# Kernel tuning notes

Hardware: AMD Instinct MI355X
Metric: run time of the kernel (lower is better)

## Reference

```python
import jax, jax.numpy as jnp
import numpy as np

D = 2048
H = 16
DH = D // H
S = 8192
EPS = 1e-6  # flax LayerNorm default


def _ln(x, g, b):
    m = jnp.mean(x, axis=-1, keepdims=True)
    v = jnp.var(x, axis=-1, keepdims=True)
    return (x - m) * jax.lax.rsqrt(v + EPS) * g + b


def setup_inputs() -> dict:
    key = jax.random.key(0)
    ks = jax.random.split(key, 12)
    sd = 1.0 / np.sqrt(D)
    sdf = 1.0 / np.sqrt(4 * D)
    return {
        "self_tok": jax.random.normal(ks[0], (D,), jnp.float32),
        "all_toks": jax.random.normal(ks[1], (S, D), jnp.float32),
        "wq": jax.random.normal(ks[2], (D, D), jnp.float32) * sd,
        "bq": jnp.zeros((D,), jnp.float32),
        "wk": jax.random.normal(ks[3], (D, D), jnp.float32) * sd,
        "bk": jnp.zeros((D,), jnp.float32),
        "wv": jax.random.normal(ks[4], (D, D), jnp.float32) * sd,
        "bv": jnp.zeros((D,), jnp.float32),
        "wo": jax.random.normal(ks[5], (D, D), jnp.float32) * sd,
        "bo": jnp.zeros((D,), jnp.float32),
        "g1": jnp.ones((D,), jnp.float32),
        "b1": jnp.zeros((D,), jnp.float32),
        "g2": jnp.ones((D,), jnp.float32),
        "b2": jnp.zeros((D,), jnp.float32),
        "w_ffn1": jax.random.normal(ks[6], (D, 4 * D), jnp.float32) * sd,
        "b_ffn1": jnp.zeros((4 * D,), jnp.float32),
        "w_ffn2": jax.random.normal(ks[7], (4 * D, D), jnp.float32) * sdf,
        "b_ffn2": jnp.zeros((D,), jnp.float32),
    }


def reference(self_tok, all_toks, wq, bq, wk, bk, wv, bv, wo, bo,
              g1, b1, g2, b2, w_ffn1, b_ffn1, w_ffn2, b_ffn2):
    # pre-norm (norm1 applied to both query token and KV tokens)
    n_self = _ln(self_tok, g1, b1)            # [D]
    n_all = _ln(all_toks, g1, b1)             # [S, D]
    q = (n_self @ wq + bq).reshape(H, DH)     # [H, Dh]
    k = (n_all @ wk + bk).reshape(S, H, DH)   # [S, H, Dh]
    v = (n_all @ wv + bv).reshape(S, H, DH)
    scale = DH ** -0.5
    scores = jnp.einsum('hd,shd->hs', q, k) * scale   # [H, S]
    attn = jax.nn.softmax(scores, axis=-1)
    out = jnp.einsum('hs,shd->hd', attn, v).reshape(D)
    out = out @ wo + bo
    x = self_tok + out
    ffn = jax.nn.gelu(_ln(x, g2, b2) @ w_ffn1 + b_ffn1) @ w_ffn2 + b_ffn2
    return x + ffn
```

## Files before the change

kernel.cpp:

```cpp
#include <hip/hip_runtime.h>

#define DEV __device__ __forceinline__

constexpr int D  = 2048;
constexpr int H  = 16;
constexpr int DH = 128;
constexpr int S  = 8192;
constexpr float EPS = 1e-6f;
constexpr float SCALE = 0.08838834764831845f;
constexpr float M0 = 8.0f;

typedef unsigned short ushortv4 __attribute__((ext_vector_type(4)));
typedef short bf16x8 __attribute__((ext_vector_type(8)));
typedef float f32x4 __attribute__((ext_vector_type(4)));

DEV float bf2f(unsigned short u){ return __uint_as_float(((unsigned int)u) << 16); }
DEV unsigned short f2bf(float f){
  unsigned int x = __float_as_uint(f);
  unsigned int r = x + 0x7fffu + ((x >> 16) & 1u);
  return (unsigned short)(r >> 16);
}

DEV float gelu(float x){
  float x3 = x * x * x;
  return 0.5f * x * (1.f + tanhf(0.7978845608028654f * (x + 0.044715f * x3)));
}

template<int NW>
DEV void block_sum2(float& a, float& b, float* buf){
  #pragma unroll
  for(int o = 32; o; o >>= 1){ a += __shfl_xor(a, o); b += __shfl_xor(b, o); }
  const int w = threadIdx.x >> 6;
  if((threadIdx.x & 63) == 0){ buf[w] = a; buf[NW + w] = b; }
  __syncthreads();
  a = buf[0]; b = buf[NW];
  #pragma unroll
  for(int i = 1; i < NW; i++){ a += buf[i]; b += buf[NW + i]; }
}

__global__ __launch_bounds__(256) void k_pre(const float* __restrict__ at,
    const float* __restrict__ g1, const float* __restrict__ b1,
    unsigned short* __restrict__ nall,
    const float* __restrict__ st, const float* __restrict__ wq,
    float* __restrict__ qpart){
  const int t = threadIdx.x;
  const int bid = blockIdx.x;
  const int w = t >> 6, l = t & 63;
  if(bid < 2048){
    const size_t s = (size_t)bid * 4 + w;
    const float4* row4 = (const float4*)(at + s * D);
    float4 a[8];
    float sum = 0.f, sq = 0.f;
    #pragma unroll
    for(int k = 0; k < 8; k++){
      a[k] = row4[l + 64 * k];
      sum += a[k].x + a[k].y + a[k].z + a[k].w;
      sq  += a[k].x*a[k].x + a[k].y*a[k].y + a[k].z*a[k].z + a[k].w*a[k].w;
    }
    #pragma unroll
    for(int o = 32; o; o >>= 1){ sum += __shfl_xor(sum, o); sq += __shfl_xor(sq, o); }
    const float m = sum * (1.f / D);
    const float r = rsqrtf(sq * (1.f / D) - m * m + EPS);
    const float4* g4 = (const float4*)g1;
    const float4* b4 = (const float4*)b1;
    ushortv4* nst = (ushortv4*)(nall + s * D);
    #pragma unroll
    for(int k = 0; k < 8; k++){
      const int j4 = l + 64 * k;
      float4 gg = g4[j4], bb = b4[j4];
      ushortv4 o4;
      o4[0] = f2bf((a[k].x - m) * r * gg.x + bb.x);
      o4[1] = f2bf((a[k].y - m) * r * gg.y + bb.y);
      o4[2] = f2bf((a[k].z - m) * r * gg.z + bb.z);
      o4[3] = f2bf((a[k].w - m) * r * gg.w + bb.w);
      nst[j4] = o4;
    }
  } else {
    __shared__ float buf[8];
    __shared__ float ns_s[32];
    const int qb_ = bid - 2048;
    const int jc = qb_ >> 3, ic = qb_ & 7;
    const int j0 = jc * 32;
    float4 a = ((const float4*)st)[t], c = ((const float4*)st)[t + 256];
    float sum = a.x + a.y + a.z + a.w + c.x + c.y + c.z + c.w;
    float sq  = a.x*a.x + a.y*a.y + a.z*a.z + a.w*a.w
              + c.x*c.x + c.y*c.y + c.z*c.z + c.w*c.w;
    block_sum2<4>(sum, sq, buf);
    const float m = sum * (1.f / D);
    const float r = rsqrtf(sq * (1.f / D) - m * m + EPS);
    if(t < 32){
      int j = j0 + t;
      ns_s[t] = (st[j] - m) * r * g1[j] + b1[j];
    }
    __syncthreads();
    const int i = ic * 256 + t;
    float acc = 0.f;
    #pragma unroll 8
    for(int jj = 0; jj < 32; jj++)
      acc = fmaf(ns_s[jj], wq[(size_t)(j0 + jj) * D + i], acc);
    qpart[(size_t)jc * D + i] = acc;
  }
}

__global__ __launch_bounds__(256) void k_qred(const float* __restrict__ qpart,
    const float* __restrict__ bq, float* __restrict__ q){
  const int i = blockIdx.x * 256 + threadIdx.x;
  float s = bq[i];
  #pragma unroll 8
  for(int p = 0; p < 64; p++) s += qpart[(size_t)p * D + i];
  q[i] = s;
}

__global__ __launch_bounds__(256) void k_wkq(const float* __restrict__ wk,
    const float* __restrict__ bk, const float* __restrict__ q,
    unsigned short* __restrict__ wkqT, float* __restrict__ qb){
  const int t = threadIdx.x;
  const int w = t >> 6, l = t & 63;
  const int row = blockIdx.x * 2 + (w >> 1);
  const int hw = w & 1;
  if(row > D) return;
  const float* src = (row < D) ? (wk + (size_t)row * D) : bk;
  const float4* s4 = (const float4*)src;
  const float4* q4 = (const float4*)q;
  float ph[4];
  #pragma unroll
  for(int kk = 0; kk < 4; kk++){
    const int kc = hw * 4 + kk;
    float4 a = s4[l + 64 * kc];
    float4 qq = q4[l + 64 * kc];
    ph[kk] = a.x*qq.x + a.y*qq.y + a.z*qq.z + a.w*qq.w;
  }
  #pragma unroll
  for(int o = 1; o < 32; o <<= 1){
    #pragma unroll
    for(int kk = 0; kk < 4; kk++) ph[kk] += __shfl_xor(ph[kk], o);
  }
  if((l & 31) == 0){
    const int hb = l >> 5;
    #pragma unroll
    for(int kk = 0; kk < 4; kk++){
      const int h = 2 * (hw * 4 + kk) + hb;
      if(row < D) wkqT[(size_t)h * D + row] = f2bf(ph[kk]);
      else        qb[h] = ph[kk];
    }
  }
}

__global__ __launch_bounds__(512) void k_scores(
    const unsigned short* __restrict__ nall,
    const unsigned short* __restrict__ wkqT,
    const float* __restrict__ qb,
    float* __restrict__ p,
    float* __restrict__ zb){
  __shared__ f32x4 cred[8][64];
  const int t = threadIdx.x;
  const int w = t >> 6, lane = t & 63;
  const int s0 = blockIdx.x * 16;
  const int m16 = lane & 15;
  const int kg  = lane >> 4;
  f32x4 c = {0.f, 0.f, 0.f, 0.f};
  const int kbase = w * 256 + kg * 8;
  const unsigned short* aptr = wkqT + (size_t)m16 * D + kbase;
  const unsigned short* bptr = nall + (size_t)(s0 + m16) * D + kbase;
  #pragma unroll
  for(int kk = 0; kk < 8; kk++){
    bf16x8 av = *(const bf16x8*)(aptr + kk * 32);
    bf16x8 bv = *(const bf16x8*)(bptr + kk * 32);
    c = __builtin_amdgcn_mfma_f32_16x16x32_bf16(av, bv, c, 0, 0, 0);
  }
  cred[w][lane] = c;
  __syncthreads();
  if(w == 0){
    f32x4 cs_ = cred[0][lane];
    #pragma unroll
    for(int pg = 1; pg < 8; pg++){
      f32x4 cp = cred[pg][lane];
      cs_[0] += cp[0]; cs_[1] += cp[1]; cs_[2] += cp[2]; cs_[3] += cp[3];
    }
    float pv[4];
    #pragma unroll
    for(int rg = 0; rg < 4; rg++)
      pv[rg] = __expf((cs_[rg] + qb[kg * 4 + rg]) * SCALE - M0);
    float4 st4;
    st4.x = pv[0]; st4.y = pv[1]; st4.z = pv[2]; st4.w = pv[3];
    *(float4*)(p + (size_t)(s0 + m16) * H + kg * 4) = st4;
    #pragma unroll
    for(int rg = 0; rg < 4; rg++){
      float e = pv[rg];
      #pragma unroll
      for(int o = 1; o < 16; o <<= 1) e += __shfl_xor(e, o);
      pv[rg] = e;
    }
    if(m16 == 0){
      float4 bz;
      bz.x = pv[0]; bz.y = pv[1]; bz.z = pv[2]; bz.w = pv[3];
      *(float4*)(zb + (size_t)blockIdx.x * H + kg * 4) = bz;
    }
  }
}

__global__ __launch_bounds__(256) void k_actx(const unsigned short* __restrict__ nall,
    const float* __restrict__ p, float* __restrict__ part){
  __shared__ float pl[64][16];
  const int jc = blockIdx.x, sc = blockIdx.y, t = threadIdx.x;
  const int s0 = sc * 64;
  #pragma unroll
  for(int u = 0; u < 4; u++){
    int idx = t + 256 * u;
    int ss = idx >> 4, hh = idx & 15;
    pl[ss][hh] = p[(size_t)(s0 + ss) * H + hh];
  }
  __syncthreads();
  const int j = jc * 512 + 2 * t;
  float acc[16][2];
  #pragma unroll
  for(int h = 0; h < 16; h++){ acc[h][0] = 0.f; acc[h][1] = 0.f; }
  for(int s8 = 0; s8 < 8; s8++){
    unsigned int nv[8];
    #pragma unroll
    for(int e = 0; e < 8; e++)
      nv[e] = *(const unsigned int*)(nall + (size_t)(s0 + s8 * 8 + e) * D + j);
    #pragma unroll
    for(int e = 0; e < 8; e++){
      const int ss = s8 * 8 + e;
      float n0 = bf2f((unsigned short)(nv[e] & 0xffffu));
      float n1 = bf2f((unsigned short)(nv[e] >> 16));
      const float4* pp = (const float4*)pl[ss];
      #pragma unroll
      for(int hq = 0; hq < 4; hq++){
        float4 p4 = pp[hq];
        acc[hq*4+0][0] = fmaf(p4.x, n0, acc[hq*4+0][0]);
        acc[hq*4+0][1] = fmaf(p4.x, n1, acc[hq*4+0][1]);
        acc[hq*4+1][0] = fmaf(p4.y, n0, acc[hq*4+1][0]);
        acc[hq*4+1][1] = fmaf(p4.y, n1, acc[hq*4+1][1]);
        acc[hq*4+2][0] = fmaf(p4.z, n0, acc[hq*4+2][0]);
        acc[hq*4+2][1] = fmaf(p4.z, n1, acc[hq*4+2][1]);
        acc[hq*4+3][0] = fmaf(p4.w, n0, acc[hq*4+3][0]);
        acc[hq*4+3][1] = fmaf(p4.w, n1, acc[hq*4+3][1]);
      }
    }
  }
  #pragma unroll
  for(int h = 0; h < 16; h++){
    float2 st2; st2.x = acc[h][0]; st2.y = acc[h][1];
    *(float2*)(part + ((size_t)sc * 16 + h) * D + j) = st2;
  }
}

__global__ __launch_bounds__(256) void k_wv(const float* __restrict__ part,
    const float* __restrict__ zb, const float* __restrict__ wv,
    float* __restrict__ part_wv){
  __shared__ float zred[16][16];
  __shared__ float ihz_s;
  __shared__ float a4[4][64];
  __shared__ float as[64];
  __shared__ float red2[2][128];
  const int h = blockIdx.x, jc = blockIdx.y, t = threadIdx.x;
  const int j0 = jc * 64;
  {
    const int hh = t & 15, u = t >> 4;
    float s = 0.f;
    #pragma unroll
    for(int k = 0; k < 32; k++) s += zb[(size_t)(u + 16 * k) * 16 + hh];
    zred[u][hh] = s;
  }
  __syncthreads();
  if(t == 0){
    float z = 0.f;
    #pragma unroll
    for(int u = 0; u < 16; u++) z += zred[u][h];
    ihz_s = 1.f / z;
  }
  const int jq = t & 63, qq = t >> 6;
  float s_ = 0.f;
  #pragma unroll
  for(int u = 0; u < 32; u++){
    int sc = qq * 32 + u;
    s_ += part[((size_t)sc * 16 + h) * D + j0 + jq];
  }
  a4[qq][jq] = s_;
  __syncthreads();
  if(t < 64) as[t] = (a4[0][t] + a4[1][t] + a4[2][t] + a4[3][t]) * ihz_s;
  __syncthreads();
  const int hf = t >> 7, il = t & 127;
  const int i = h * DH + il;
  float acc = 0.f;
  #pragma unroll
  for(int u = 0; u < 32; u++){
    int jj = hf * 32 + u;
    acc = fmaf(as[jj], wv[(size_t)(j0 + jj) * D + i], acc);
  }
  red2[hf][il] = acc;
  __syncthreads();
  if(t < 128) part_wv[(size_t)jc * D + h * DH + t] = red2[0][t] + red2[1][t];
}

__global__ __launch_bounds__(256) void k_wo(const float* __restrict__ part_wv,
    const float* __restrict__ bv, const float* __restrict__ wo,
    float* __restrict__ part_wo){
  __shared__ float oa[32];
  const int ic = blockIdx.x, jc = blockIdx.y, t = threadIdx.x;
  const int j0 = jc * 32;
  if(t < 32){
    float s = bv[j0 + t];
    #pragma unroll
    for(int pg = 0; pg < 32; pg++) s += part_wv[(size_t)pg * D + j0 + t];
    oa[t] = s;
  }
  __syncthreads();
  const int i = ic * 256 + t;
  float acc = 0.f;
  #pragma unroll
  for(int jj = 0; jj < 32; jj++)
    acc = fmaf(oa[jj], wo[(size_t)(j0 + jj) * D + i], acc);
  part_wo[(size_t)jc * D + i] = acc;
}

__global__ __launch_bounds__(256) void k_x(const float* __restrict__ self_tok,
    const float* __restrict__ bo, const float* __restrict__ part_wo,
    float* __restrict__ x, float* __restrict__ xstat){
  __shared__ float buf[8];
  const int b = blockIdx.x, t = threadIdx.x;
  const int i = b * 256 + t;
  float s = self_tok[i] + bo[i];
  #pragma unroll 8
  for(int pg = 0; pg < 64; pg++) s += part_wo[(size_t)pg * D + i];
  x[i] = s;
  float sq = s * s;
  block_sum2<4>(s, sq, buf);
  if(t == 0){ xstat[2 * b] = s; xstat[2 * b + 1] = sq; }
}

__global__ __launch_bounds__(256) void k_f1(const float* __restrict__ x,
    const float* __restrict__ xstat, const float* __restrict__ g2,
    const float* __restrict__ b2, const float* __restrict__ w1,
    float* __restrict__ part_f1){
  __shared__ float xs[128];
  __shared__ float stat[2];
  const int oc = blockIdx.x, jc = blockIdx.y, t = threadIdx.x;
  if(t == 0){
    float s1 = 0.f, s2 = 0.f;
    #pragma unroll
    for(int pg = 0; pg < 8; pg++){ s1 += xstat[2 * pg]; s2 += xstat[2 * pg + 1]; }
    float m = s1 * (1.f / D);
    stat[0] = m;
    stat[1] = rsqrtf(s2 * (1.f / D) - m * m + EPS);
  }
  __syncthreads();
  if(t < 128){
    int j = jc * 128 + t;
    xs[t] = (x[j] - stat[0]) * stat[1] * g2[j] + b2[j];
  }
  __syncthreads();
  const int o = oc * 256 + t;
  float acc = 0.f;
  #pragma unroll 8
  for(int jj = 0; jj < 128; jj++)
    acc = fmaf(xs[jj], w1[(size_t)(jc * 128 + jj) * (4 * D) + o], acc);
  part_f1[(size_t)jc * (4 * D) + o] = acc;
}

__global__ __launch_bounds__(256) void k_f2(const float* __restrict__ part_f1,
    const float* __restrict__ b_f1, const float* __restrict__ w2,
    float* __restrict__ part_f2){
  __shared__ float hs[128];
  const int ic = blockIdx.x, jc = blockIdx.y, t = threadIdx.x;
  if(t < 128){
    int jh = jc * 128 + t;
    float s = b_f1[jh];
    #pragma unroll
    for(int pg = 0; pg < 16; pg++) s += part_f1[(size_t)pg * (4 * D) + jh];
    hs[t] = gelu(s);
  }
  __syncthreads();
  const int i = ic * 256 + t;
  float acc = 0.f;
  #pragma unroll 8
  for(int jj = 0; jj < 128; jj++)
    acc = fmaf(hs[jj], w2[(size_t)(jc * 128 + jj) * D + i], acc);
  part_f2[(size_t)jc * D + i] = acc;
}

__global__ __launch_bounds__(256) void k_final(const float* __restrict__ part_f2,
    const float* __restrict__ x, const float* __restrict__ b_f2,
    float* __restrict__ out){
  const int i = blockIdx.x * 256 + threadIdx.x;
  float s = x[i] + b_f2[i];
  #pragma unroll 8
  for(int jc = 0; jc < 64; jc++) s += part_f2[(size_t)jc * D + i];
  out[i] = s;
}

extern "C" void kernel_launch(void* const* d_in, const int* in_sizes, int n_in,
                              void* d_out, int out_size, void* d_ws, size_t ws_size,
                              hipStream_t stream){
  const float* self_tok = (const float*)d_in[0];
  const float* all_toks = (const float*)d_in[1];
  const float* wq = (const float*)d_in[2];
  const float* bq = (const float*)d_in[3];
  const float* wk = (const float*)d_in[4];
  const float* bk = (const float*)d_in[5];
  const float* wv = (const float*)d_in[6];
  const float* bv = (const float*)d_in[7];
  const float* wo = (const float*)d_in[8];
  const float* bo = (const float*)d_in[9];
  const float* g1 = (const float*)d_in[10];
  const float* b1 = (const float*)d_in[11];
  const float* g2 = (const float*)d_in[12];
  const float* b2 = (const float*)d_in[13];
  const float* w1 = (const float*)d_in[14];
  const float* b_f1 = (const float*)d_in[15];
  const float* w2 = (const float*)d_in[16];
  const float* b_f2 = (const float*)d_in[17];
  float* out = (float*)d_out;

  char* wptr = (char*)d_ws;
  auto alloc = [&](size_t bytes) -> void* {
    void* pt = (void*)wptr;
    wptr += (bytes + 255) & ~(size_t)255;
    return pt;
  };
  unsigned short* n_all = (unsigned short*)alloc((size_t)S * D * 2);
  unsigned short* wkqT  = (unsigned short*)alloc((size_t)H * D * 2);
  float* pbuf      = (float*)alloc((size_t)S * H * 4);
  float* zb        = (float*)alloc((size_t)(S / 16) * H * 4);
  float* qpart     = (float*)alloc((size_t)64 * D * 4);
  float* q         = (float*)alloc((size_t)D * 4);
  float* qb        = (float*)alloc(64);
  float* part_actx = (float*)alloc((size_t)128 * H * D * 4);
  float* part_wv   = (float*)alloc((size_t)32 * D * 4);
  float* part_wo   = (float*)alloc((size_t)64 * D * 4);
  float* xbuf      = (float*)alloc((size_t)D * 4);
  float* xstat     = (float*)alloc(64);
  float* part_f1   = (float*)alloc((size_t)16 * 4 * D * 4);
  float* part_f2   = (float*)alloc((size_t)64 * D * 4);

  k_pre<<<2048 + 512, 256, 0, stream>>>(all_toks, g1, b1, n_all, self_tok, wq, qpart);
  k_qred<<<8, 256, 0, stream>>>(qpart, bq, q);
  k_wkq<<<(D / 2) + 1, 256, 0, stream>>>(wk, bk, q, wkqT, qb);
  k_scores<<<S / 16, 512, 0, stream>>>(n_all, wkqT, qb, pbuf, zb);
  k_actx<<<dim3(4, 128), 256, 0, stream>>>(n_all, pbuf, part_actx);
  k_wv<<<dim3(16, 32), 256, 0, stream>>>(part_actx, zb, wv, part_wv);
  k_wo<<<dim3(8, 64), 256, 0, stream>>>(part_wv, bv, wo, part_wo);
  k_x<<<8, 256, 0, stream>>>(self_tok, bo, part_wo, xbuf, xstat);
  k_f1<<<dim3(32, 16), 256, 0, stream>>>(xbuf, xstat, g2, b2, w1, part_f1);
  k_f2<<<dim3(8, 64), 256, 0, stream>>>(part_f1, b_f1, w2, part_f2);
  k_final<<<8, 256, 0, stream>>>(part_f2, xbuf, b_f2, out);
}
```

Measured before the change: 116.0 us.

## Re-split FFN GEMVs with float4 loads and parallelize partial-sum reductions

The FFN GEMV kernels now use float4 weight loads with 32-row K chunks, so there are more K-split blocks (64 for f1, 256 for f2) and each thread computes 4 outputs. The reduction kernels (q, f2 input, final) split each column's partial sums across 8 thread groups and combine them through shared memory, running 64 blocks instead of 8. The aim is more memory-level parallelism and better occupancy on the weight-streaming and reduction phases. In exchange the partial-sum buffers grow, so more intermediate data is written and read back.

```diff
diff --git a/kernel.cpp b/kernel.cpp
--- a/kernel.cpp
+++ b/kernel.cpp
@@ -104,11 +104,22 @@
 
 __global__ __launch_bounds__(256) void k_qred(const float* __restrict__ qpart,
     const float* __restrict__ bq, float* __restrict__ q){
-  const int i = blockIdx.x * 256 + threadIdx.x;
-  float s = bq[i];
-  #pragma unroll 8
-  for(int p = 0; p < 64; p++) s += qpart[(size_t)p * D + i];
-  q[i] = s;
+  __shared__ float red[8][32];
+  const int b = blockIdx.x, t = threadIdx.x;
+  const int il = t & 31, pg8 = t >> 5;
+  const int i = b * 32 + il;
+  float s = 0.f;
+  #pragma unroll
+  for(int k = 0; k < 8; k++) s += qpart[(size_t)(pg8 * 8 + k) * D + i];
+  red[pg8][il] = s;
+  __syncthreads();
+  if(t < 32){
+    const int i2 = b * 32 + t;
+    float v = bq[i2];
+    #pragma unroll
+    for(int p = 0; p < 8; p++) v += red[p][t];
+    q[i2] = v;
+  }
 }
 
 __global__ __launch_bounds__(256) void k_wkq(const float* __restrict__ wk,
@@ -335,60 +346,87 @@
     const float* __restrict__ xstat, const float* __restrict__ g2,
     const float* __restrict__ b2, const float* __restrict__ w1,
     float* __restrict__ part_f1){
-  __shared__ float xs[128];
-  __shared__ float stat[2];
+  __shared__ float xs[32];
   const int oc = blockIdx.x, jc = blockIdx.y, t = threadIdx.x;
-  if(t == 0){
+  if(t < 32){
     float s1 = 0.f, s2 = 0.f;
     #pragma unroll
     for(int pg = 0; pg < 8; pg++){ s1 += xstat[2 * pg]; s2 += xstat[2 * pg + 1]; }
-    float m = s1 * (1.f / D);
-    stat[0] = m;
-    stat[1] = rsqrtf(s2 * (1.f / D) - m * m + EPS);
-  }
-  __syncthreads();
-  if(t < 128){
-    int j = jc * 128 + t;
-    xs[t] = (x[j] - stat[0]) * stat[1] * g2[j] + b2[j];
-  }
-  __syncthreads();
-  const int o = oc * 256 + t;
-  float acc = 0.f;
+    const float m = s1 * (1.f / D);
+    const float r = rsqrtf(s2 * (1.f / D) - m * m + EPS);
+    const int j = jc * 32 + t;
+    xs[t] = (x[j] - m) * r * g2[j] + b2[j];
+  }
+  __syncthreads();
+  const int o = oc * 1024 + 4 * t;
+  float4 acc = {0.f, 0.f, 0.f, 0.f};
   #pragma unroll 8
-  for(int jj = 0; jj < 128; jj++)
-    acc = fmaf(xs[jj], w1[(size_t)(jc * 128 + jj) * (4 * D) + o], acc);
-  part_f1[(size_t)jc * (4 * D) + o] = acc;
+  for(int jj = 0; jj < 32; jj++){
+    float4 w4 = *(const float4*)(w1 + (size_t)(jc * 32 + jj) * (4 * D) + o);
+    const float xv = xs[jj];
+    acc.x = fmaf(xv, w4.x, acc.x);
+    acc.y = fmaf(xv, w4.y, acc.y);
+    acc.z = fmaf(xv, w4.z, acc.z);
+    acc.w = fmaf(xv, w4.w, acc.w);
+  }
+  *(float4*)(part_f1 + (size_t)jc * (4 * D) + o) = acc;
 }
 
 __global__ __launch_bounds__(256) void k_f2(const float* __restrict__ part_f1,
     const float* __restrict__ b_f1, const float* __restrict__ w2,
     float* __restrict__ part_f2){
-  __shared__ float hs[128];
-  const int ic = blockIdx.x, jc = blockIdx.y, t = threadIdx.x;
-  if(t < 128){
-    int jh = jc * 128 + t;
-    float s = b_f1[jh];
-    #pragma unroll
-    for(int pg = 0; pg < 16; pg++) s += part_f1[(size_t)pg * (4 * D) + jh];
-    hs[t] = gelu(s);
-  }
-  __syncthreads();
-  const int i = ic * 256 + t;
-  float acc = 0.f;
+  __shared__ float red[8][32];
+  __shared__ float hs[32];
+  const int ic = blockIdx.x, jc2 = blockIdx.y, t = threadIdx.x;
+  const int jh_l = t & 31, pg8 = t >> 5;
+  {
+    float s = 0.f;
+    #pragma unroll
+    for(int k = 0; k < 8; k++)
+      s += part_f1[(size_t)(pg8 * 8 + k) * (4 * D) + jc2 * 32 + jh_l];
+    red[pg8][jh_l] = s;
+  }
+  __syncthreads();
+  if(t < 32){
+    float v = b_f1[jc2 * 32 + t];
+    #pragma unroll
+    for(int pg = 0; pg < 8; pg++) v += red[pg][t];
+    hs[t] = gelu(v);
+  }
+  __syncthreads();
+  const int i = ic * 1024 + 4 * t;
+  float4 acc = {0.f, 0.f, 0.f, 0.f};
   #pragma unroll 8
-  for(int jj = 0; jj < 128; jj++)
-    acc = fmaf(hs[jj], w2[(size_t)(jc * 128 + jj) * D + i], acc);
-  part_f2[(size_t)jc * D + i] = acc;
+  for(int jj = 0; jj < 32; jj++){
+    float4 w4 = *(const float4*)(w2 + (size_t)(jc2 * 32 + jj) * D + i);
+    const float hv = hs[jj];
+    acc.x = fmaf(hv, w4.x, acc.x);
+    acc.y = fmaf(hv, w4.y, acc.y);
+    acc.z = fmaf(hv, w4.z, acc.z);
+    acc.w = fmaf(hv, w4.w, acc.w);
+  }
+  *(float4*)(part_f2 + (size_t)jc2 * D + i) = acc;
 }
 
 __global__ __launch_bounds__(256) void k_final(const float* __restrict__ part_f2,
     const float* __restrict__ x, const float* __restrict__ b_f2,
     float* __restrict__ out){
-  const int i = blockIdx.x * 256 + threadIdx.x;
-  float s = x[i] + b_f2[i];
+  __shared__ float red[8][32];
+  const int b = blockIdx.x, t = threadIdx.x;
+  const int il = t & 31, pg8 = t >> 5;
+  const int i = b * 32 + il;
+  float s = 0.f;
   #pragma unroll 8
-  for(int jc = 0; jc < 64; jc++) s += part_f2[(size_t)jc * D + i];
-  out[i] = s;
+  for(int k = 0; k < 32; k++) s += part_f2[(size_t)(pg8 * 32 + k) * D + i];
+  red[pg8][il] = s;
+  __syncthreads();
+  if(t < 32){
+    const int i2 = b * 32 + t;
+    float v = x[i2] + b_f2[i2];
+    #pragma unroll
+    for(int pg = 0; pg < 8; pg++) v += red[pg][t];
+    out[i2] = v;
+  }
 }
 
 extern "C" void kernel_launch(void* const* d_in, const int* in_sizes, int n_in,
@@ -432,18 +470,18 @@
   float* part_wo   = (float*)alloc((size_t)64 * D * 4);
   float* xbuf      = (float*)alloc((size_t)D * 4);
   float* xstat     = (float*)alloc(64);
-  float* part_f1   = (float*)alloc((size_t)16 * 4 * D * 4);
-  float* part_f2   = (float*)alloc((size_t)64 * D * 4);
+  float* part_f1   = (float*)alloc((size_t)64 * 4 * D * 4);
+  float* part_f2   = (float*)alloc((size_t)256 * D * 4);
 
   k_pre<<<2048 + 512, 256, 0, stream>>>(all_toks, g1, b1, n_all, self_tok, wq, qpart);
-  k_qred<<<8, 256, 0, stream>>>(qpart, bq, q);
+  k_qred<<<64, 256, 0, stream>>>(qpart, bq, q);
   k_wkq<<<(D / 2) + 1, 256, 0, stream>>>(wk, bk, q, wkqT, qb);
   k_scores<<<S / 16, 512, 0, stream>>>(n_all, wkqT, qb, pbuf, zb);
   k_actx<<<dim3(4, 128), 256, 0, stream>>>(n_all, pbuf, part_actx);
   k_wv<<<dim3(16, 32), 256, 0, stream>>>(part_actx, zb, wv, part_wv);
   k_wo<<<dim3(8, 64), 256, 0, stream>>>(part_wv, bv, wo, part_wo);
   k_x<<<8, 256, 0, stream>>>(self_tok, bo, part_wo, xbuf, xstat);
-  k_f1<<<dim3(32, 16), 256, 0, stream>>>(xbuf, xstat, g2, b2, w1, part_f1);
-  k_f2<<<dim3(8, 64), 256, 0, stream>>>(part_f1, b_f1, w2, part_f2);
-  k_final<<<8, 256, 0, stream>>>(part_f2, xbuf, b_f2, out);
-}
+  k_f1<<<dim3(8, 64), 256, 0, stream>>>(xbuf, xstat, g2, b2, w1, part_f1);
+  k_f2<<<dim3(2, 256), 256, 0, stream>>>(part_f1, b_f1, w2, part_f2);
+  k_final<<<64, 256, 0, stream>>>(part_f2, xbuf, b_f2, out);
+}
```

Result: faster. 106.7 us (-8.0%).
